# Kernel optimization log

Hardware: AMD Instinct MI355X
Metric: run time of the kernel (lower is better)

Reference implementation:

```python
import jax, jax.numpy as jnp
import numpy as np

B, C, D, H, W = 2, 128, 16, 64, 64

def setup_inputs() -> dict:
    key = jax.random.key(0)
    x = jax.random.normal(key, (B, C, D, H, W), dtype=jnp.float32)
    gamma = jnp.zeros((1,), dtype=jnp.float32)
    return {"x": x, "gamma": gamma}

def reference(x, gamma):
    b, c, d, h, w = x.shape
    n = d * h * w
    q = x.reshape(b, c, n)                      # proj_query: B x C x N
    # energy = Q @ K^T where K = Q (same tensor, transposed): B x C x C
    energy = jnp.einsum('bcn,bkn->bck', q, q)
    # max-subtraction trick: energy_new = max(energy, -1) - energy, then softmax
    energy_new = jnp.max(energy, axis=-1, keepdims=True) - energy
    attention = jax.nn.softmax(energy_new, axis=-1)  # B x C x C
    out = jnp.einsum('bck,bkn->bcn', attention, q)   # AV
    out = out.reshape(b, c, d, h, w)
    return gamma * out + x
```

## Files before the change

### kernel.cpp

```cpp
#include <hip/hip_runtime.h>
#include <hip/hip_bf16.h>
#include <stdint.h>

#define BB  2
#define CC  128
#define NNN 65536

typedef __bf16 bf16x8 __attribute__((ext_vector_type(8)));
typedef float  f32x16 __attribute__((ext_vector_type(16)));

__device__ __forceinline__ uint16_t f2bf(float f) {
    uint32_t u = __float_as_uint(f);
    u = (u + 0x7fffu + ((u >> 16) & 1u)) >> 16;
    return (uint16_t)u;
}
__device__ __forceinline__ uint32_t pack2(float a, float b) {
    return (uint32_t)f2bf(a) | ((uint32_t)f2bf(b) << 16);
}

#define GCH  256
#define GST  64
#define GPAD 130

__global__ __launch_bounds__(256) void gram_kernel(const float* __restrict__ x,
        uint16_t* __restrict__ qT, float* __restrict__ partial) {
    const int bid = blockIdx.x;
    const int b   = bid >> 8, chunk = bid & 255;
    const int n0  = chunk * GCH;
    const int t   = threadIdx.x;
    const int w = t >> 6, l = t & 63, h = l >> 5, ln = l & 31;

    __shared__ uint4 lds[2][8 * GPAD];

    const float* xb = x + (size_t)b * CC * NNN;

    const int sc = t >> 3;
    const int sg = t & 7;

    f32x16 acc[4];
#pragma unroll
    for (int j = 0; j < 4; ++j)
#pragma unroll
        for (int r = 0; r < 16; ++r) acc[j][r] = 0.0f;

    float4 va[4], vb[4];
#pragma unroll
    for (int p = 0; p < 4; ++p) {
        const float* gp = xb + (size_t)(sc + 32 * p) * NNN + n0 + sg * 8;
        va[p] = *(const float4*)(gp);
        vb[p] = *(const float4*)(gp + 4);
    }

    for (int st = 0; st < 4; ++st) {
        const int buf = st & 1;
#pragma unroll
        for (int p = 0; p < 4; ++p) {
            uint4 u;
            u.x = pack2(va[p].x, va[p].y);
            u.y = pack2(va[p].z, va[p].w);
            u.z = pack2(vb[p].x, vb[p].y);
            u.w = pack2(vb[p].z, vb[p].w);
            lds[buf][sg * GPAD + sc + 32 * p] = u;
        }
        if (st < 3) {
#pragma unroll
            for (int p = 0; p < 4; ++p) {
                const float* gp = xb + (size_t)(sc + 32 * p) * NNN + n0 + (st + 1) * GST + sg * 8;
                va[p] = *(const float4*)(gp);
                vb[p] = *(const float4*)(gp + 4);
            }
        }
        __syncthreads();

#pragma unroll
        for (int s = 0; s < 4; ++s) {
            bf16x8 fa = *(const bf16x8*)&lds[buf][(2 * s + h) * GPAD + 32 * w + ln];
#pragma unroll
            for (int j = 0; j < 4; ++j) {
                bf16x8 fb = *(const bf16x8*)&lds[buf][(2 * s + h) * GPAD + 32 * j + ln];
                acc[j] = __builtin_amdgcn_mfma_f32_32x32x16_bf16(fa, fb, acc[j], 0, 0, 0);
            }
        }

        {
            const int rn = t >> 2;
            const int cs = (t & 3) * 32;
            const int gg = rn >> 3, sub = rn & 7;
            const uint16_t* lu = (const uint16_t*)&lds[buf][0];
            uint32_t ow[16];
#pragma unroll
            for (int k2 = 0; k2 < 16; ++k2) {
                uint32_t lo = lu[(gg * GPAD + cs + 2 * k2) * 8 + sub];
                uint32_t hi = lu[(gg * GPAD + cs + 2 * k2 + 1) * 8 + sub];
                ow[k2] = lo | (hi << 16);
            }
            uint16_t* qrow = qT + ((size_t)b * NNN + n0 + st * GST + rn) * CC + cs;
            *(uint4*)(qrow + 0)  = *(uint4*)&ow[0];
            *(uint4*)(qrow + 8)  = *(uint4*)&ow[4];
            *(uint4*)(qrow + 16) = *(uint4*)&ow[8];
            *(uint4*)(qrow + 24) = *(uint4*)&ow[12];
        }
    }

    float* pb = partial + (size_t)bid * (CC * CC);
#pragma unroll
    for (int j = 0; j < 4; ++j)
#pragma unroll
        for (int r = 0; r < 16; ++r) {
            int row = 32 * w + (r & 3) + 8 * (r >> 2) + 4 * h;
            pb[row * CC + 32 * j + ln] = acc[j][r];
        }
}

__global__ __launch_bounds__(256) void reduce_softmax_kernel(
        const float* __restrict__ partial, const float* __restrict__ gamma,
        uint16_t* __restrict__ attw) {
    const int row = blockIdx.x;
    const int b = row >> 7, i = row & 127;
    const int t = threadIdx.x;
    const int j = t & 127, ph = t >> 7;

    const float* base = partial + ((size_t)(b * 256 + ph * 128)) * (CC * CC)
                      + (size_t)i * CC + j;
    float s0=0,s1=0,s2=0,s3=0,s4=0,s5=0,s6=0,s7=0;
    for (int p = 0; p < 128; p += 8) {
        s0 += base[(size_t)(p + 0) * (CC * CC)];
        s1 += base[(size_t)(p + 1) * (CC * CC)];
        s2 += base[(size_t)(p + 2) * (CC * CC)];
        s3 += base[(size_t)(p + 3) * (CC * CC)];
        s4 += base[(size_t)(p + 4) * (CC * CC)];
        s5 += base[(size_t)(p + 5) * (CC * CC)];
        s6 += base[(size_t)(p + 6) * (CC * CC)];
        s7 += base[(size_t)(p + 7) * (CC * CC)];
    }
    const float sp = ((s0 + s1) + (s2 + s3)) + ((s4 + s5) + (s6 + s7));

    __shared__ float red[256];
    __shared__ float m[128];
    red[t] = sp; __syncthreads();
    const float e = red[j] + red[j + 128];

    if (ph == 0) m[j] = e;
    __syncthreads();
    for (int s = 64; s > 0; s >>= 1) {
        if (ph == 0 && j < s) m[j] = fmaxf(m[j], m[j + s]);
        __syncthreads();
    }
    const float M = m[0]; __syncthreads();
    const float v = M - e;
    if (ph == 0) m[j] = v;
    __syncthreads();
    for (int s = 64; s > 0; s >>= 1) {
        if (ph == 0 && j < s) m[j] = fmaxf(m[j], m[j + s]);
        __syncthreads();
    }
    const float m2 = m[0]; __syncthreads();
    const float pexp = __expf(v - m2);
    if (ph == 0) m[j] = pexp;
    __syncthreads();
    for (int s = 64; s > 0; s >>= 1) {
        if (ph == 0 && j < s) m[j] += m[j + s];
        __syncthreads();
    }
    const float sum = m[0];

    if (ph == 0)
        attw[(size_t)row * CC + j] = f2bf(gamma[0] * pexp / sum);
}

#define AV_NB 256
__global__ __launch_bounds__(256) void av_kernel(const uint16_t* __restrict__ qT,
        const uint16_t* __restrict__ attw, const float* __restrict__ x,
        float* __restrict__ out) {
    const int b     = blockIdx.y;
    const int nbase = blockIdx.x * AV_NB;
    const int t = threadIdx.x;
    const int w = t >> 6, l = t & 63, h = l >> 5, ln = l & 31;

    __shared__ uint4 attL[16 * 129];
    __shared__ uint4 qTL[2][16 * 33];

    {
        const uint16_t* ab = attw + (size_t)b * CC * CC;
#pragma unroll
        for (int p = 0; p < 8; ++p) {
            int c = p * 16 + (t >> 4), g = t & 15;
            attL[g * 129 + c] = *(const uint4*)(ab + (size_t)c * CC + g * 8);
        }
    }
    const uint16_t* qTb = qT + (size_t)b * NNN * CC;
    {
#pragma unroll
        for (int p = 0; p < 2; ++p) {
            int nn = p * 16 + (t >> 4), g = t & 15;
            qTL[0][g * 33 + nn] = *(const uint4*)(qTb + (size_t)(nbase + nn) * CC + g * 8);
        }
    }

    const size_t obase0 = ((size_t)b * CC + 32 * w) * NNN + nbase + ln;
    const int iters = AV_NB / 32;

    for (int it = 0; it < iters; ++it) {
        __syncthreads();
        const size_t ob = obase0 + it * 32;
        float xr[16];
#pragma unroll
        for (int r = 0; r < 16; ++r) {
            int row = (r & 3) + 8 * (r >> 2) + 4 * h;
            xr[r] = x[ob + (size_t)row * NNN];
        }
        uint4 sv0, sv1;
        if (it + 1 < iters) {
            int g = t & 15;
            sv0 = *(const uint4*)(qTb + (size_t)(nbase + (it + 1) * 32 + (t >> 4)) * CC + g * 8);
            sv1 = *(const uint4*)(qTb + (size_t)(nbase + (it + 1) * 32 + 16 + (t >> 4)) * CC + g * 8);
        }
        f32x16 acc;
#pragma unroll
        for (int r = 0; r < 16; ++r) acc[r] = 0.0f;
        const int buf = it & 1;
#pragma unroll
        for (int s = 0; s < 8; ++s) {
            bf16x8 fa = *(const bf16x8*)&attL[(2 * s + h) * 129 + 32 * w + ln];
            bf16x8 fb = *(const bf16x8*)&qTL[buf][(2 * s + h) * 33 + ln];
            acc = __builtin_amdgcn_mfma_f32_32x32x16_bf16(fa, fb, acc, 0, 0, 0);
        }
        if (it + 1 < iters) {
            int g = t & 15;
            qTL[1 - buf][g * 33 + (t >> 4)]      = sv0;
            qTL[1 - buf][g * 33 + 16 + (t >> 4)] = sv1;
        }
#pragma unroll
        for (int r = 0; r < 16; ++r) {
            int row = (r & 3) + 8 * (r >> 2) + 4 * h;
            out[ob + (size_t)row * NNN] = acc[r] + xr[r];
        }
    }
}

extern "C" void kernel_launch(void* const* d_in, const int* in_sizes, int n_in,
                              void* d_out, int out_size, void* d_ws, size_t ws_size,
                              hipStream_t stream) {
    const float* x     = (const float*)d_in[0];
    const float* gamma = (const float*)d_in[1];
    float* out = (float*)d_out;

    uint16_t* qT      = (uint16_t*)d_ws;
    float*    partial = (float*)(qT + (size_t)BB * NNN * CC);
    uint16_t* att     = (uint16_t*)(partial + (size_t)512 * CC * CC);

    gram_kernel<<<BB * (NNN / GCH), 256, 0, stream>>>(x, qT, partial);
    reduce_softmax_kernel<<<BB * CC, 256, 0, stream>>>(partial, gamma, att);
    av_kernel<<<dim3(NNN / AV_NB, BB), 256, 0, stream>>>(qT, att, x, out);
}
```

Measured before the change: 158.4 us.

## Drop bf16 transposed Q intermediate; AV kernel reads x directly into swizzled LDS

The gram kernel no longer writes a transposed bf16 copy of the input (qT) to global memory. The AV kernel now loads x tiles itself, converts them to bf16 into an XOR-swizzled LDS tile, and computes the full 128x128 output tile with four MFMA accumulators per wave. The gram prefetch is also deepened to two stages. This removes a 32 MB write and its later read, in exchange for re-reading fp32 x in the AV pass, scalar 16-bit LDS gathers to build B fragments, and a large 32 KB LDS tile that may limit occupancy.

New measurement: 153.3 us. 3.2% less time.

```diff
diff --git a/kernel.cpp b/kernel.cpp
--- a/kernel.cpp
+++ b/kernel.cpp
@@ -23,7 +23,7 @@
 #define GPAD 130
 
 __global__ __launch_bounds__(256) void gram_kernel(const float* __restrict__ x,
-        uint16_t* __restrict__ qT, float* __restrict__ partial) {
+        float* __restrict__ partial) {
     const int bid = blockIdx.x;
     const int b   = bid >> 8, chunk = bid & 255;
     const int n0  = chunk * GCH;
@@ -33,7 +33,6 @@
     __shared__ uint4 lds[2][8 * GPAD];
 
     const float* xb = x + (size_t)b * CC * NNN;
-
     const int sc = t >> 3;
     const int sg = t & 7;
 
@@ -43,62 +42,44 @@
 #pragma unroll
         for (int r = 0; r < 16; ++r) acc[j][r] = 0.0f;
 
-    float4 va[4], vb[4];
-#pragma unroll
-    for (int p = 0; p < 4; ++p) {
-        const float* gp = xb + (size_t)(sc + 32 * p) * NNN + n0 + sg * 8;
-        va[p] = *(const float4*)(gp);
-        vb[p] = *(const float4*)(gp + 4);
-    }
+    float4 va[2][4], vb[2][4];
+#pragma unroll
+    for (int s2 = 0; s2 < 2; ++s2)
+#pragma unroll
+        for (int p = 0; p < 4; ++p) {
+            const float* gp = xb + (size_t)(sc + 32 * p) * NNN + n0 + s2 * GST + sg * 8;
+            va[s2][p] = *(const float4*)(gp);
+            vb[s2][p] = *(const float4*)(gp + 4);
+        }
 
     for (int st = 0; st < 4; ++st) {
-        const int buf = st & 1;
+        const int set = st & 1;
 #pragma unroll
         for (int p = 0; p < 4; ++p) {
             uint4 u;
-            u.x = pack2(va[p].x, va[p].y);
-            u.y = pack2(va[p].z, va[p].w);
-            u.z = pack2(vb[p].x, vb[p].y);
-            u.w = pack2(vb[p].z, vb[p].w);
-            lds[buf][sg * GPAD + sc + 32 * p] = u;
-        }
-        if (st < 3) {
+            u.x = pack2(va[set][p].x, va[set][p].y);
+            u.y = pack2(va[set][p].z, va[set][p].w);
+            u.z = pack2(vb[set][p].x, vb[set][p].y);
+            u.w = pack2(vb[set][p].z, vb[set][p].w);
+            lds[set][sg * GPAD + sc + 32 * p] = u;
+        }
+        if (st + 2 < 4) {
 #pragma unroll
             for (int p = 0; p < 4; ++p) {
-                const float* gp = xb + (size_t)(sc + 32 * p) * NNN + n0 + (st + 1) * GST + sg * 8;
-                va[p] = *(const float4*)(gp);
-                vb[p] = *(const float4*)(gp + 4);
+                const float* gp = xb + (size_t)(sc + 32 * p) * NNN + n0 + (st + 2) * GST + sg * 8;
+                va[set][p] = *(const float4*)(gp);
+                vb[set][p] = *(const float4*)(gp + 4);
             }
         }
         __syncthreads();
-
 #pragma unroll
         for (int s = 0; s < 4; ++s) {
-            bf16x8 fa = *(const bf16x8*)&lds[buf][(2 * s + h) * GPAD + 32 * w + ln];
+            bf16x8 fa = *(const bf16x8*)&lds[set][(2 * s + h) * GPAD + 32 * w + ln];
 #pragma unroll
             for (int j = 0; j < 4; ++j) {
-                bf16x8 fb = *(const bf16x8*)&lds[buf][(2 * s + h) * GPAD + 32 * j + ln];
+                bf16x8 fb = *(const bf16x8*)&lds[set][(2 * s + h) * GPAD + 32 * j + ln];
                 acc[j] = __builtin_amdgcn_mfma_f32_32x32x16_bf16(fa, fb, acc[j], 0, 0, 0);
             }
-        }
-
-        {
-            const int rn = t >> 2;
-            const int cs = (t & 3) * 32;
-            const int gg = rn >> 3, sub = rn & 7;
-            const uint16_t* lu = (const uint16_t*)&lds[buf][0];
-            uint32_t ow[16];
-#pragma unroll
-            for (int k2 = 0; k2 < 16; ++k2) {
-                uint32_t lo = lu[(gg * GPAD + cs + 2 * k2) * 8 + sub];
-                uint32_t hi = lu[(gg * GPAD + cs + 2 * k2 + 1) * 8 + sub];
-                ow[k2] = lo | (hi << 16);
-            }
-            uint16_t* qrow = qT + ((size_t)b * NNN + n0 + st * GST + rn) * CC + cs;
-            *(uint4*)(qrow + 0)  = *(uint4*)&ow[0];
-            *(uint4*)(qrow + 8)  = *(uint4*)&ow[4];
-            *(uint4*)(qrow + 16) = *(uint4*)&ow[8];
-            *(uint4*)(qrow + 24) = *(uint4*)&ow[12];
         }
     }
 
@@ -168,74 +149,75 @@
         attw[(size_t)row * CC + j] = f2bf(gamma[0] * pexp / sum);
 }
 
-#define AV_NB 256
-__global__ __launch_bounds__(256) void av_kernel(const uint16_t* __restrict__ qT,
-        const uint16_t* __restrict__ attw, const float* __restrict__ x,
-        float* __restrict__ out) {
-    const int b     = blockIdx.y;
-    const int nbase = blockIdx.x * AV_NB;
-    const int t = threadIdx.x;
+#define AVN 128
+
+union FB8 { uint16_t u[8]; bf16x8 v; };
+
+__global__ __launch_bounds__(256) void av_kernel(const float* __restrict__ x,
+        const uint16_t* __restrict__ attw, float* __restrict__ out) {
+    const int b  = blockIdx.y;
+    const int n0 = blockIdx.x * AVN;
+    const int t  = threadIdx.x;
     const int w = t >> 6, l = t & 63, h = l >> 5, ln = l & 31;
 
-    __shared__ uint4 attL[16 * 129];
-    __shared__ uint4 qTL[2][16 * 33];
+    __shared__ uint4    attL[16 * 128];
+    __shared__ uint16_t xL[128 * 128];
 
     {
         const uint16_t* ab = attw + (size_t)b * CC * CC;
 #pragma unroll
         for (int p = 0; p < 8; ++p) {
             int c = p * 16 + (t >> 4), g = t & 15;
-            attL[g * 129 + c] = *(const uint4*)(ab + (size_t)c * CC + g * 8);
-        }
-    }
-    const uint16_t* qTb = qT + (size_t)b * NNN * CC;
+            attL[g * 128 + c] = *(const uint4*)(ab + (size_t)c * CC + g * 8);
+        }
+    }
     {
-#pragma unroll
-        for (int p = 0; p < 2; ++p) {
-            int nn = p * 16 + (t >> 4), g = t & 15;
-            qTL[0][g * 33 + nn] = *(const uint4*)(qTb + (size_t)(nbase + nn) * CC + g * 8);
-        }
-    }
-
-    const size_t obase0 = ((size_t)b * CC + 32 * w) * NNN + nbase + ln;
-    const int iters = AV_NB / 32;
-
-    for (int it = 0; it < iters; ++it) {
-        __syncthreads();
-        const size_t ob = obase0 + it * 32;
-        float xr[16];
+        const int kr = t >> 1, nh = (t & 1) * 64;
+        const int sw = ((kr & 8) << 2) | ((kr & 7) << 3);
+        const float* xr = x + ((size_t)b * CC + kr) * NNN + n0 + nh;
+#pragma unroll
+        for (int i = 0; i < 8; ++i) {
+            float4 a  = *(const float4*)(xr + i * 8);
+            float4 bq = *(const float4*)(xr + i * 8 + 4);
+            uint4 u;
+            u.x = pack2(a.x, a.y);  u.y = pack2(a.z, a.w);
+            u.z = pack2(bq.x, bq.y); u.w = pack2(bq.z, bq.w);
+            *(uint4*)&xL[kr * 128 + ((nh + i * 8) ^ sw)] = u;
+        }
+    }
+    __syncthreads();
+
+    f32x16 acc[4];
+#pragma unroll
+    for (int jt = 0; jt < 4; ++jt)
+#pragma unroll
+        for (int r = 0; r < 16; ++r) acc[jt][r] = 0.0f;
+
+#pragma unroll
+    for (int s = 0; s < 8; ++s) {
+        bf16x8 fa = *(const bf16x8*)&attL[(2 * s + h) * 128 + 32 * w + ln];
+        const int k0 = s * 16 + h * 8;
+#pragma unroll
+        for (int jt = 0; jt < 4; ++jt) {
+            FB8 fb;
+#pragma unroll
+            for (int jj = 0; jj < 8; ++jj) {
+                const int k = k0 + jj;
+                const int sw = ((k & 8) << 2) | ((k & 7) << 3);
+                fb.u[jj] = xL[k * 128 + ((32 * jt + ln) ^ sw)];
+            }
+            acc[jt] = __builtin_amdgcn_mfma_f32_32x32x16_bf16(fa, fb.v, acc[jt], 0, 0, 0);
+        }
+    }
+
+#pragma unroll
+    for (int jt = 0; jt < 4; ++jt)
 #pragma unroll
         for (int r = 0; r < 16; ++r) {
             int row = (r & 3) + 8 * (r >> 2) + 4 * h;
-            xr[r] = x[ob + (size_t)row * NNN];
-        }
-        uint4 sv0, sv1;
-        if (it + 1 < iters) {
-            int g = t & 15;
-            sv0 = *(const uint4*)(qTb + (size_t)(nbase + (it + 1) * 32 + (t >> 4)) * CC + g * 8);
-            sv1 = *(const uint4*)(qTb + (size_t)(nbase + (it + 1) * 32 + 16 + (t >> 4)) * CC + g * 8);
-        }
-        f32x16 acc;
-#pragma unroll
-        for (int r = 0; r < 16; ++r) acc[r] = 0.0f;
-        const int buf = it & 1;
-#pragma unroll
-        for (int s = 0; s < 8; ++s) {
-            bf16x8 fa = *(const bf16x8*)&attL[(2 * s + h) * 129 + 32 * w + ln];
-            bf16x8 fb = *(const bf16x8*)&qTL[buf][(2 * s + h) * 33 + ln];
-            acc = __builtin_amdgcn_mfma_f32_32x32x16_bf16(fa, fb, acc, 0, 0, 0);
-        }
-        if (it + 1 < iters) {
-            int g = t & 15;
-            qTL[1 - buf][g * 33 + (t >> 4)]      = sv0;
-            qTL[1 - buf][g * 33 + 16 + (t >> 4)] = sv1;
-        }
-#pragma unroll
-        for (int r = 0; r < 16; ++r) {
-            int row = (r & 3) + 8 * (r >> 2) + 4 * h;
-            out[ob + (size_t)row * NNN] = acc[r] + xr[r];
-        }
-    }
+            size_t off = ((size_t)b * CC + 32 * w + row) * NNN + n0 + 32 * jt + ln;
+            out[off] = acc[jt][r] + x[off];
+        }
 }
 
 extern "C" void kernel_launch(void* const* d_in, const int* in_sizes, int n_in,
@@ -245,11 +227,10 @@
     const float* gamma = (const float*)d_in[1];
     float* out = (float*)d_out;
 
-    uint16_t* qT      = (uint16_t*)d_ws;
-    float*    partial = (float*)(qT + (size_t)BB * NNN * CC);
+    float*    partial = (float*)d_ws;
     uint16_t* att     = (uint16_t*)(partial + (size_t)512 * CC * CC);
 
-    gram_kernel<<<BB * (NNN / GCH), 256, 0, stream>>>(x, qT, partial);
+    gram_kernel<<<BB * (NNN / GCH), 256, 0, stream>>>(x, partial);
     reduce_softmax_kernel<<<BB * CC, 256, 0, stream>>>(partial, gamma, att);
-    av_kernel<<<dim3(NNN / AV_NB, BB), 256, 0, stream>>>(qT, att, x, out);
-}
+    av_kernel<<<dim3(NNN / AVN, BB), 256, 0, stream>>>(x, att, out);
+}
```
